# Kernel tuning notes

Hardware: AMD Instinct MI355X
Metric: run time of the kernel (lower is better)

The kernel has to match this reference:

```python
import jax, jax.numpy as jnp
import numpy as np
from jax import lax

B, S, DIMS, T, K = 4, 4096, 2048, 10, 2


def setup_inputs() -> dict:
    key = jax.random.key(0)
    ks = jax.random.split(key, 4)
    scale = 1.0 / np.sqrt(DIMS)
    x = jax.random.normal(ks[0], (B, S, DIMS), dtype=jnp.float32)
    W_cls = jax.random.normal(ks[1], (DIMS, T), dtype=jnp.float32) * scale
    W_sparse = jax.random.normal(ks[2], (DIMS, T), dtype=jnp.float32) * scale
    W_gates = jax.random.normal(ks[3], (DIMS, T), dtype=jnp.float32) * scale
    return {
        "x": x,
        "W_cls": W_cls, "b_cls": jnp.zeros((T,), jnp.float32),
        "W_sparse": W_sparse, "b_sparse": jnp.zeros((T,), jnp.float32),
        "W_gates": W_gates, "b_gates": jnp.zeros((T,), jnp.float32),
        "alpha": jnp.ones((1,), jnp.float32),
    }


def reference(x, W_cls, b_cls, W_sparse, b_sparse, W_gates, b_gates, alpha):
    # soft routing: softmax classifier over num_types
    soft_types = jax.nn.softmax(jnp.einsum("bsd,dt->bst", x, W_cls) + b_cls, axis=-1)
    # sparse routing: top-k over logits, softmax over the k kept logits,
    # scattered back into a dense [B,S,T] gate vector (zeros elsewhere)
    logits = jnp.einsum("bsd,dt->bst", x, W_sparse) + b_sparse
    top_v, top_i = lax.top_k(logits, K)                      # [B,S,K]
    sparse_g = jax.nn.softmax(top_v, axis=-1)                # [B,S,K]
    # scatter via one-hot (K and T are tiny)
    sparse_types = jnp.sum(jax.nn.one_hot(top_i, T, dtype=x.dtype) * sparse_g[..., None], axis=-2)  # [B,S,T]
    # per-type sigmoid gates: batched single matmul == stack of Linear(dims,1)+Sigmoid
    gates = jax.nn.sigmoid(jnp.einsum("bsd,dt->bst", x, W_gates) + b_gates)  # [B,S,T]
    a = jax.nn.sigmoid(alpha)                                # [1], broadcasts
    mixed_types = a * sparse_types + (1.0 - a) * soft_types  # [B,S,T]
    # original: gates stacked as [B,S,1,T], mixed unsqueezed to [B,S,1,T], sum over T -> [B,S,1]
    return jnp.sum(gates * mixed_types, axis=-1, keepdims=True)
```

## Files before the change

### kernel.cpp

```cpp
#include <hip/hip_runtime.h>
#include <math.h>
#include <stdint.h>


#define NROWS   16384
#define DIMS_   2048
#define TT      10

typedef __attribute__((ext_vector_type(8))) short short8;
typedef __attribute__((ext_vector_type(4))) float f32x4;

__device__ __forceinline__ unsigned short bf16_rne(float f) {
    unsigned int u = __float_as_uint(f);
    unsigned int r = u + 0x7fffu + ((u >> 16) & 1u);
    return (unsigned short)(r >> 16);
}

__global__ __launch_bounds__(256)
void tgate_k0(const float* __restrict__ W_cls,
              const float* __restrict__ W_sparse,
              const float* __restrict__ W_gates,
              unsigned short* __restrict__ frag)
{
    int t = blockIdx.x * 256 + threadIdx.x;
    int K0   = t >> 7;
    int nt   = (t >> 6) & 1;
    int lane = t & 63;
    int n  = nt * 16 + (lane & 15);
    int kb = K0 * 32 + (lane >> 4) * 8;
    short8 hi, lo;
    #pragma unroll
    for (int j = 0; j < 8; ++j) {
        int k = kb + j;
        float w = 0.0f;
        if (n < 10)      w = W_cls[k * TT + n];
        else if (n < 20) w = W_sparse[k * TT + n - 10];
        else if (n < 30) w = W_gates[k * TT + n - 20];
        unsigned short h = bf16_rne(w);
        float back = __uint_as_float(((unsigned int)h) << 16);
        hi[j] = (short)h;
        lo[j] = (short)bf16_rne(w - back);
    }
    short8* fv = reinterpret_cast<short8*>(frag);
    fv[(K0 * 4 + nt * 2 + 0) * 64 + lane] = hi;
    fv[(K0 * 4 + nt * 2 + 1) * 64 + lane] = lo;
}

__device__ __forceinline__ void issue_chunk(const float* __restrict__ x,
                                            float* bufbase, int row0, int lane,
                                            int colf0)
{
    #pragma unroll
    for (int t = 0; t < 4; ++t) {
        const float* gp = x + (size_t)(row0 + 4 * t + (lane >> 4)) * DIMS_
                            + colf0 + (lane & 15) * 4;
        __builtin_amdgcn_global_load_lds(
            (const __attribute__((address_space(1))) void*)gp,
            (__attribute__((address_space(3))) void*)(bufbase + t * 260),
            16, 0, 2);
    }
}

__device__ __forceinline__ void compute_chunk(const float* Lbuf,
                                              const short8* __restrict__ fv,
                                              int K0b, int lane, int m, int quad,
                                              f32x4& accA, f32x4& accB)
{
    #pragma unroll
    for (int ksl = 0; ksl < 2; ++ksl) {
        const int K0 = K0b + ksl;
        const float* src = Lbuf + (m >> 2) * 260 + (m & 3) * 64 + ksl * 32 + quad * 8;
        float4 b0 = *reinterpret_cast<const float4*>(src);
        float4 b1 = *reinterpret_cast<const float4*>(src + 4);
        float f[8] = {b0.x, b0.y, b0.z, b0.w, b1.x, b1.y, b1.z, b1.w};
        short8 ah, al;
        #pragma unroll
        for (int j = 0; j < 8; ++j) {
            unsigned short hh = bf16_rne(f[j]);
            float back = __uint_as_float(((unsigned int)hh) << 16);
            ah[j] = (short)hh;
            al[j] = (short)bf16_rne(f[j] - back);
        }
        short8 fh0 = fv[(K0 * 4 + 0) * 64 + lane];
        short8 fl0 = fv[(K0 * 4 + 1) * 64 + lane];
        short8 fh1 = fv[(K0 * 4 + 2) * 64 + lane];
        short8 fl1 = fv[(K0 * 4 + 3) * 64 + lane];
        accA = __builtin_amdgcn_mfma_f32_16x16x32_bf16(ah, fh0, accA, 0, 0, 0);
        accA = __builtin_amdgcn_mfma_f32_16x16x32_bf16(al, fh0, accA, 0, 0, 0);
        accA = __builtin_amdgcn_mfma_f32_16x16x32_bf16(ah, fl0, accA, 0, 0, 0);
        accB = __builtin_amdgcn_mfma_f32_16x16x32_bf16(ah, fh1, accB, 0, 0, 0);
        accB = __builtin_amdgcn_mfma_f32_16x16x32_bf16(al, fh1, accB, 0, 0, 0);
        accB = __builtin_amdgcn_mfma_f32_16x16x32_bf16(ah, fl1, accB, 0, 0, 0);
    }
}

__global__ __launch_bounds__(256)
void tgate_k1(const float* __restrict__ x,
              const unsigned short* __restrict__ frag,
              const float* __restrict__ b_cls,
              const float* __restrict__ b_sparse,
              const float* __restrict__ b_gates,
              const float* __restrict__ alpha,
              float* __restrict__ out)
{
    __shared__ alignas(16) float lds[4][2][1040];

    const int tid   = threadIdx.x;
    const int lane  = tid & 63;
    const int wv    = __builtin_amdgcn_readfirstlane(tid >> 6);
    const int row0  = blockIdx.x * 16;
    const int m     = lane & 15;
    const int quad  = lane >> 4;
    const int cbase = wv * 512;

    float* B0 = &lds[wv][0][0];
    float* B1 = &lds[wv][1][0];
    const short8* fv = reinterpret_cast<const short8*>(frag);

    f32x4 acc[2][2];
    #pragma unroll
    for (int h = 0; h < 2; ++h) {
        acc[h][0] = (f32x4){0.f, 0.f, 0.f, 0.f};
        acc[h][1] = (f32x4){0.f, 0.f, 0.f, 0.f};
    }

    __builtin_amdgcn_sched_barrier(0);
    issue_chunk(x, B0, row0, lane, cbase + 0 * 64);
    issue_chunk(x, B1, row0, lane, cbase + 1 * 64);

    for (int c = 0; c < 4; ++c) {
        __builtin_amdgcn_s_waitcnt(0x0F74);
        float* buf = (c & 1) ? B1 : B0;
        compute_chunk(buf, fv, 16 * wv + 2 * c, lane, m, quad, acc[0][0], acc[0][1]);
        __builtin_amdgcn_sched_barrier(0);
        issue_chunk(x, buf, row0, lane, cbase + (c + 2) * 64);
    }
    for (int c = 4; c < 6; ++c) {
        __builtin_amdgcn_s_waitcnt(0x0F74);
        float* buf = (c & 1) ? B1 : B0;
        compute_chunk(buf, fv, 16 * wv + 2 * c, lane, m, quad, acc[1][0], acc[1][1]);
        __builtin_amdgcn_sched_barrier(0);
        issue_chunk(x, buf, row0, lane, cbase + (c + 2) * 64);
    }
    __builtin_amdgcn_s_waitcnt(0x0F74);
    compute_chunk(B0, fv, 16 * wv + 12, lane, m, quad, acc[1][0], acc[1][1]);
    __builtin_amdgcn_s_waitcnt(0x0F70);
    compute_chunk(B1, fv, 16 * wv + 14, lane, m, quad, acc[1][0], acc[1][1]);

    float* red = &lds[0][0][0];
    __syncthreads();
    #pragma unroll
    for (int h = 0; h < 2; ++h) {
        int s = 2 * wv + h;
        #pragma unroll
        for (int r = 0; r < 4; ++r) {
            int row = quad * 4 + r;
            red[(s * 16 + row) * 33 + m]      = acc[h][0][r];
            red[(s * 16 + row) * 33 + m + 16] = acc[h][1][r];
        }
    }
    __syncthreads();

    float* fold = red + 8 * 16 * 33;
    #pragma unroll
    for (int u = 0; u < 2; ++u) {
        int i = tid * 2 + u;
        int row = i >> 5, j = i & 31;
        float a = 0.0f;
        #pragma unroll
        for (int s = 0; s < 8; ++s) a += red[(s * 16 + row) * 33 + j];
        fold[row * 33 + j] = a;
    }
    __syncthreads();

    if (tid < 16) {
        const float* l = &fold[tid * 33];
        float lc[TT], lsp[TT], g[TT];
        #pragma unroll
        for (int t = 0; t < TT; ++t) {
            lc[t]  = l[t]      + b_cls[t];
            lsp[t] = l[10 + t] + b_sparse[t];
            float lg = l[20 + t] + b_gates[t];
            g[t] = 1.0f / (1.0f + __expf(-lg));
        }
        float mm = lc[0];
        #pragma unroll
        for (int t = 1; t < TT; ++t) mm = fmaxf(mm, lc[t]);
        float esum = 0.0f, gdot = 0.0f;
        #pragma unroll
        for (int t = 0; t < TT; ++t) {
            float e = __expf(lc[t] - mm);
            esum += e;
            gdot = fmaf(g[t], e, gdot);
        }
        float v1 = lsp[0], v2 = -1e30f, gv1 = g[0], gv2 = 0.0f;
        #pragma unroll
        for (int t = 1; t < TT; ++t) {
            if (lsp[t] > v1)      { v2 = v1; gv2 = gv1; v1 = lsp[t]; gv1 = g[t]; }
            else if (lsp[t] > v2) { v2 = lsp[t]; gv2 = g[t]; }
        }
        float s1 = 1.0f / (1.0f + __expf(v2 - v1));
        float s2 = 1.0f - s1;
        float a  = 1.0f / (1.0f + __expf(-alpha[0]));
        float sparse_dot = fmaf(gv1, s1, gv2 * s2);
        out[row0 + tid] = fmaf(a, sparse_dot, (1.0f - a) * (gdot / esum));
    }
}

extern "C" void kernel_launch(void* const* d_in, const int* in_sizes, int n_in,
                              void* d_out, int out_size, void* d_ws, size_t ws_size,
                              hipStream_t stream) {
    const float* x        = (const float*)d_in[0];
    const float* W_cls    = (const float*)d_in[1];
    const float* b_cls    = (const float*)d_in[2];
    const float* W_sparse = (const float*)d_in[3];
    const float* b_sparse = (const float*)d_in[4];
    const float* W_gates  = (const float*)d_in[5];
    const float* b_gates  = (const float*)d_in[6];
    const float* alpha    = (const float*)d_in[7];
    float* out = (float*)d_out;

    unsigned short* frag = (unsigned short*)d_ws;

    tgate_k0<<<dim3(32), dim3(256), 0, stream>>>(W_cls, W_sparse, W_gates, frag);
    tgate_k1<<<dim3(NROWS / 16), dim3(256), 0, stream>>>(x, frag, b_cls, b_sparse,
                                                         b_gates, alpha, out);
}
```

Before: 204.5 us.

## Load x directly into registers with a 3-deep software pipeline instead of LDS staging

Drops the global_load_lds double-buffered staging of x through shared memory. Each lane now loads its own fragment of x straight into registers, along with the weight fragments, using a register ring buffer three stages deep, fully unrolled over 16 K-steps. This removes the LDS write/read round trip and the waitcnt choreography, and shrinks LDS to just the reduction buffer, which may allow more resident blocks. The cost is higher register pressure, and each lane's global reads are 32-byte pieces scattered across rows, so coalescing may be worse than the previous row-contiguous 16-byte loads.

```diff
diff --git a/kernel.cpp b/kernel.cpp
--- a/kernel.cpp
+++ b/kernel.cpp
@@ -6,6 +6,7 @@
 #define NROWS   16384
 #define DIMS_   2048
 #define TT      10
+#define PIPE_D  3
 
 typedef __attribute__((ext_vector_type(8))) short short8;
 typedef __attribute__((ext_vector_type(4))) float f32x4;
@@ -46,54 +47,6 @@
     fv[(K0 * 4 + nt * 2 + 1) * 64 + lane] = lo;
 }
 
-__device__ __forceinline__ void issue_chunk(const float* __restrict__ x,
-                                            float* bufbase, int row0, int lane,
-                                            int colf0)
-{
-    #pragma unroll
-    for (int t = 0; t < 4; ++t) {
-        const float* gp = x + (size_t)(row0 + 4 * t + (lane >> 4)) * DIMS_
-                            + colf0 + (lane & 15) * 4;
-        __builtin_amdgcn_global_load_lds(
-            (const __attribute__((address_space(1))) void*)gp,
-            (__attribute__((address_space(3))) void*)(bufbase + t * 260),
-            16, 0, 2);
-    }
-}
-
-__device__ __forceinline__ void compute_chunk(const float* Lbuf,
-                                              const short8* __restrict__ fv,
-                                              int K0b, int lane, int m, int quad,
-                                              f32x4& accA, f32x4& accB)
-{
-    #pragma unroll
-    for (int ksl = 0; ksl < 2; ++ksl) {
-        const int K0 = K0b + ksl;
-        const float* src = Lbuf + (m >> 2) * 260 + (m & 3) * 64 + ksl * 32 + quad * 8;
-        float4 b0 = *reinterpret_cast<const float4*>(src);
-        float4 b1 = *reinterpret_cast<const float4*>(src + 4);
-        float f[8] = {b0.x, b0.y, b0.z, b0.w, b1.x, b1.y, b1.z, b1.w};
-        short8 ah, al;
-        #pragma unroll
-        for (int j = 0; j < 8; ++j) {
-            unsigned short hh = bf16_rne(f[j]);
-            float back = __uint_as_float(((unsigned int)hh) << 16);
-            ah[j] = (short)hh;
-            al[j] = (short)bf16_rne(f[j] - back);
-        }
-        short8 fh0 = fv[(K0 * 4 + 0) * 64 + lane];
-        short8 fl0 = fv[(K0 * 4 + 1) * 64 + lane];
-        short8 fh1 = fv[(K0 * 4 + 2) * 64 + lane];
-        short8 fl1 = fv[(K0 * 4 + 3) * 64 + lane];
-        accA = __builtin_amdgcn_mfma_f32_16x16x32_bf16(ah, fh0, accA, 0, 0, 0);
-        accA = __builtin_amdgcn_mfma_f32_16x16x32_bf16(al, fh0, accA, 0, 0, 0);
-        accA = __builtin_amdgcn_mfma_f32_16x16x32_bf16(ah, fl0, accA, 0, 0, 0);
-        accB = __builtin_amdgcn_mfma_f32_16x16x32_bf16(ah, fh1, accB, 0, 0, 0);
-        accB = __builtin_amdgcn_mfma_f32_16x16x32_bf16(al, fh1, accB, 0, 0, 0);
-        accB = __builtin_amdgcn_mfma_f32_16x16x32_bf16(ah, fl1, accB, 0, 0, 0);
-    }
-}
-
 __global__ __launch_bounds__(256)
 void tgate_k1(const float* __restrict__ x,
               const unsigned short* __restrict__ frag,
@@ -103,7 +56,7 @@
               const float* __restrict__ alpha,
               float* __restrict__ out)
 {
-    __shared__ alignas(16) float lds[4][2][1040];
+    __shared__ alignas(16) float red_lds[8 * 16 * 33 + 16 * 33];
 
     const int tid   = threadIdx.x;
     const int lane  = tid & 63;
@@ -113,9 +66,9 @@
     const int quad  = lane >> 4;
     const int cbase = wv * 512;
 
-    float* B0 = &lds[wv][0][0];
-    float* B1 = &lds[wv][1][0];
-    const short8* fv = reinterpret_cast<const short8*>(frag);
+    const short8* fv    = reinterpret_cast<const short8*>(frag);
+    const short8* fbase = fv + (16 * wv * 4) * 64 + lane;
+    const float*  xrow  = x + (size_t)(row0 + m) * DIMS_ + cbase + quad * 8;
 
     f32x4 acc[2][2];
     #pragma unroll
@@ -124,31 +77,55 @@
         acc[h][1] = (f32x4){0.f, 0.f, 0.f, 0.f};
     }
 
-    __builtin_amdgcn_sched_barrier(0);
-    issue_chunk(x, B0, row0, lane, cbase + 0 * 64);
-    issue_chunk(x, B1, row0, lane, cbase + 1 * 64);
-
-    for (int c = 0; c < 4; ++c) {
-        __builtin_amdgcn_s_waitcnt(0x0F74);
-        float* buf = (c & 1) ? B1 : B0;
-        compute_chunk(buf, fv, 16 * wv + 2 * c, lane, m, quad, acc[0][0], acc[0][1]);
-        __builtin_amdgcn_sched_barrier(0);
-        issue_chunk(x, buf, row0, lane, cbase + (c + 2) * 64);
-    }
-    for (int c = 4; c < 6; ++c) {
-        __builtin_amdgcn_s_waitcnt(0x0F74);
-        float* buf = (c & 1) ? B1 : B0;
-        compute_chunk(buf, fv, 16 * wv + 2 * c, lane, m, quad, acc[1][0], acc[1][1]);
-        __builtin_amdgcn_sched_barrier(0);
-        issue_chunk(x, buf, row0, lane, cbase + (c + 2) * 64);
-    }
-    __builtin_amdgcn_s_waitcnt(0x0F74);
-    compute_chunk(B0, fv, 16 * wv + 12, lane, m, quad, acc[1][0], acc[1][1]);
-    __builtin_amdgcn_s_waitcnt(0x0F70);
-    compute_chunk(B1, fv, 16 * wv + 14, lane, m, quad, acc[1][0], acc[1][1]);
-
-    float* red = &lds[0][0][0];
-    __syncthreads();
+    float4 xa[PIPE_D], xb[PIPE_D];
+    short8 fh0[PIPE_D], fl0[PIPE_D], fh1[PIPE_D], fl1[PIPE_D];
+
+    #pragma unroll
+    for (int p = 0; p < PIPE_D; ++p) {
+        fh0[p] = fbase[(p * 4 + 0) * 64];
+        fl0[p] = fbase[(p * 4 + 1) * 64];
+        fh1[p] = fbase[(p * 4 + 2) * 64];
+        fl1[p] = fbase[(p * 4 + 3) * 64];
+        xa[p]  = *reinterpret_cast<const float4*>(xrow + p * 32);
+        xb[p]  = *reinterpret_cast<const float4*>(xrow + p * 32 + 4);
+    }
+
+    #pragma unroll
+    for (int k = 0; k < 16; ++k) {
+        const int sl = k % PIPE_D;
+        const int h  = k >> 3;
+
+        float f[8] = {xa[sl].x, xa[sl].y, xa[sl].z, xa[sl].w,
+                      xb[sl].x, xb[sl].y, xb[sl].z, xb[sl].w};
+        short8 ah, al;
+        #pragma unroll
+        for (int j = 0; j < 8; ++j) {
+            unsigned short hh = bf16_rne(f[j]);
+            float back = __uint_as_float(((unsigned int)hh) << 16);
+            ah[j] = (short)hh;
+            al[j] = (short)bf16_rne(f[j] - back);
+        }
+        short8 h0 = fh0[sl], l0 = fl0[sl], h1 = fh1[sl], l1 = fl1[sl];
+
+        acc[h][0] = __builtin_amdgcn_mfma_f32_16x16x32_bf16(ah, h0, acc[h][0], 0, 0, 0);
+        acc[h][0] = __builtin_amdgcn_mfma_f32_16x16x32_bf16(al, h0, acc[h][0], 0, 0, 0);
+        acc[h][0] = __builtin_amdgcn_mfma_f32_16x16x32_bf16(ah, l0, acc[h][0], 0, 0, 0);
+        acc[h][1] = __builtin_amdgcn_mfma_f32_16x16x32_bf16(ah, h1, acc[h][1], 0, 0, 0);
+        acc[h][1] = __builtin_amdgcn_mfma_f32_16x16x32_bf16(al, h1, acc[h][1], 0, 0, 0);
+        acc[h][1] = __builtin_amdgcn_mfma_f32_16x16x32_bf16(ah, l1, acc[h][1], 0, 0, 0);
+
+        if (k + PIPE_D < 16) {
+            const int kn = k + PIPE_D;
+            fh0[sl] = fbase[(kn * 4 + 0) * 64];
+            fl0[sl] = fbase[(kn * 4 + 1) * 64];
+            fh1[sl] = fbase[(kn * 4 + 2) * 64];
+            fl1[sl] = fbase[(kn * 4 + 3) * 64];
+            xa[sl]  = *reinterpret_cast<const float4*>(xrow + kn * 32);
+            xb[sl]  = *reinterpret_cast<const float4*>(xrow + kn * 32 + 4);
+        }
+    }
+
+    float* red = red_lds;
     #pragma unroll
     for (int h = 0; h < 2; ++h) {
         int s = 2 * wv + h;
```

Result: slower. 210.9 us (+3.1%).
